# Optimization experiments

Hardware: AMD Instinct MI355X
Metric: run time of the kernel (lower is better)

Reference implementation:

```python
import jax, jax.numpy as jnp
import numpy as np

EMBED_DIM = 768
NUM_HEADS = 12
HEAD_DIM = EMBED_DIM // NUM_HEADS
SCALE = HEAD_DIM ** -0.5


def setup_inputs() -> dict:
    key = jax.random.key(0)
    k1, k2, k3, k4, k5 = jax.random.split(key, 5)
    B, T = 8, 1024
    init = 0.02
    return {
        "hidden_states": jax.random.normal(k1, (B, T, EMBED_DIM), dtype=jnp.float32),
        "qkv_w": jax.random.normal(k2, (EMBED_DIM, 3 * EMBED_DIM), dtype=jnp.float32) * init,
        "qkv_b": jnp.zeros((3 * EMBED_DIM,), dtype=jnp.float32),
        "proj_w": jax.random.normal(k3, (EMBED_DIM, EMBED_DIM), dtype=jnp.float32) * init,
        "proj_b": jnp.zeros((EMBED_DIM,), dtype=jnp.float32),
    }


def reference(hidden_states, qkv_w, qkv_b, proj_w, proj_b):
    B, T, E = hidden_states.shape
    # fused QKV projection: [B, T, 3E] -> [3, B, H, T, Dh]
    mixed = hidden_states @ qkv_w + qkv_b
    mixed = mixed.reshape(B, T, 3, NUM_HEADS, HEAD_DIM).transpose(2, 0, 3, 1, 4)
    q, k, v = mixed[0], mixed[1], mixed[2]
    # scores: [B, H, T, T]
    scores = jnp.einsum("bhqd,bhkd->bhqk", q, k) * SCALE
    probs = jax.nn.softmax(scores, axis=-1)
    # context: [B, T, H, Dh] -> [B, T, E]
    ctx = jnp.einsum("bhqk,bhkd->bqhd", probs, v).reshape(B, T, E)
    return ctx @ proj_w + proj_b
```

## Files before the change

### kernel.cpp

```cpp
#include <hip/hip_runtime.h>
#include <hip/hip_bf16.h>

#define B_ 8
#define T_ 1024
#define E_ 768
#define H_ 12
#define DH_ 64
#define E3_ 2304
#define M_ (B_ * T_)
#define SCALE_LOG2E 0.18033688011112042f

typedef __attribute__((ext_vector_type(8))) short short8;
typedef __attribute__((ext_vector_type(4))) float float4_;
typedef __attribute__((ext_vector_type(4))) unsigned short ushort4_;

__device__ __forceinline__ unsigned short f2bf(float f) {
    union { float f; unsigned int u; } v; v.f = f;
    unsigned int r = v.u + 0x7fffu + ((v.u >> 16) & 1u);
    return (unsigned short)(r >> 16);
}

__device__ __forceinline__ unsigned int pk_bf16(float a, float b) {
    float2 t; t.x = a; t.y = b;
    union { __hip_bfloat162 h; unsigned int u; } cv;
    cv.h = __float22bfloat162_rn(t);
    return cv.u;
}

__device__ __forceinline__ void gld_lds16(const unsigned short* g, unsigned short* l) {
    __builtin_amdgcn_global_load_lds(
        (const __attribute__((address_space(1))) void*)g,
        (__attribute__((address_space(3))) void*)l,
        16, 0, 0);
}

__global__ __launch_bounds__(256) void prep(const float* __restrict__ hs,
                                            const float* __restrict__ qkv_w,
                                            const float* __restrict__ proj_w,
                                            unsigned short* __restrict__ hs_bf,
                                            unsigned short* __restrict__ qkvwT,
                                            unsigned short* __restrict__ projwT) {
    __shared__ float tile[32][33];
    const int id = blockIdx.x;
    const int tid = threadIdx.x;
    if (id < 6144) {
        const int i = (id * 256 + tid) * 4;
        float4_ v = *(const float4_*)(hs + i);
        ushort4_ o;
        o.x = f2bf(v.x); o.y = f2bf(v.y); o.z = f2bf(v.z); o.w = f2bf(v.w);
        *(ushort4_*)(hs_bf + i) = o;
        return;
    }
    const float* W; unsigned short* Wt; int N, bx, by;
    if (id < 6144 + 1728) {
        const int t = id - 6144; W = qkv_w; Wt = qkvwT; N = E3_;
        bx = t % 72; by = t / 72;
    } else {
        const int t = id - 7872; W = proj_w; Wt = projwT; N = E_;
        bx = t % 24; by = t / 24;
    }
    const int k0 = by * 32, n0 = bx * 32;
    const int tx = tid & 31, ty = tid >> 5;
    for (int i = ty; i < 32; i += 8)
        tile[i][tx] = W[(size_t)(k0 + i) * N + n0 + tx];
    __syncthreads();
    for (int i = ty; i < 32; i += 8)
        Wt[(size_t)(n0 + i) * E_ + k0 + tx] = f2bf(tile[tx][i]);
}

__global__ __launch_bounds__(512, 2) void gemm288(const unsigned short* __restrict__ A,
                                                  const unsigned short* __restrict__ Wt,
                                                  const float* __restrict__ bias,
                                                  unsigned short* __restrict__ mixedOut,
                                                  unsigned short* __restrict__ Vt) {
    const int K = 768;
    const int NT = 12;
    __shared__ __align__(16) unsigned short lds[70144];

    const int tid = threadIdx.x;
    const int lane = tid & 63;
    const int w = tid >> 6;
    const int quad = lane >> 4;
    const int l16 = lane & 15;
    const int wM = w >> 1;
    const int wN = w & 1;

    const int id = blockIdx.x;
    const int xcd = id & 7;
    const int slot = id >> 3;
    const int bx = slot >> 2;
    const int byl = slot & 3;
    const int bm = (xcd * 4 + byl) * 256;
    const int bn = bx * 288;

    const int j4 = (w < 4) ? (w + 32) : 36;
    int kk0 = ((w % 18) / 6) * 64 + w;
    int kk1 = (((w + 8) % 18) / 6) * 64 + (w + 8);
    int kk2 = (((w + 16) % 18) / 6) * 64 + (w + 16);
    int kk3 = (((w + 24) % 18) / 6) * 64 + (w + 24);
    int kk4 = (j4 >= 36) ? (3 * 64 + 36) : (((j4 % 18) / 6) * 64 + j4);
#define CS_(a, b) { int _lo = min(a, b), _hi = max(a, b); a = _lo; b = _hi; }
    CS_(kk0, kk1) CS_(kk3, kk4) CS_(kk2, kk4) CS_(kk2, kk3) CS_(kk1, kk4)
    CS_(kk0, kk3) CS_(kk0, kk2) CS_(kk1, kk3) CS_(kk1, kk2)
#undef CS_
    const int b0 = kk0 & 63, b1 = kk1 & 63, b2 = kk2 & 63, b3 = kk3 & 63, b4 = kk4 & 63;

    const int srcrow = lane >> 3;
    const int ssw = ((lane & 7) ^ (srcrow & 7)) << 3;
    const unsigned short* gaL = A + (size_t)(bm + srcrow) * K + ssw;
    const unsigned short* gbL = Wt + (size_t)(bn + srcrow) * K + ssw;
    unsigned short* ldsl = lds + lane * 8;

    const int rsw0 = ((quad) ^ (l16 & 7)) << 3;
    const int rsw1 = ((quad + 4) ^ (l16 & 7)) << 3;
    const unsigned short* rdA = lds + (wM * 64 + l16) * 64;
    const unsigned short* rdB = lds + 32768 + (wN * 144 + l16) * 64;

    short8 aF[4][2], bF[3][2];
    float4_ acc[4][9] = {};

#define STA_(aj, toff, bufA) gld_lds16(gaL + (size_t)(aj) * 6144 + (toff), (bufA) + (aj) * 512)
#define STB_(j, toff, bufB) { \
    const int _j = (j); \
    const unsigned short* _s = gbL + (size_t)(_j >= 36 ? 0 : _j) * 6144 + (toff); \
    unsigned short* _d = (_j >= 36) ? (ldsl + 69632) : ((bufB) + _j * 512); \
    gld_lds16(_s, _d); }

#define LDA_(buf) { \
    const unsigned short* _a = rdA + (buf) * 16384; \
    aF[0][0] = *(const short8*)(_a + rsw0);        aF[0][1] = *(const short8*)(_a + rsw1); \
    aF[1][0] = *(const short8*)(_a + 1024 + rsw0); aF[1][1] = *(const short8*)(_a + 1024 + rsw1); \
    aF[2][0] = *(const short8*)(_a + 2048 + rsw0); aF[2][1] = *(const short8*)(_a + 2048 + rsw1); \
    aF[3][0] = *(const short8*)(_a + 3072 + rsw0); aF[3][1] = *(const short8*)(_a + 3072 + rsw1); }

#define LDB_(buf, nh) { \
    const unsigned short* _b = rdB + (buf) * 18432 + (nh) * 3072; \
    bF[0][0] = *(const short8*)(_b + rsw0);        bF[0][1] = *(const short8*)(_b + rsw1); \
    bF[1][0] = *(const short8*)(_b + 1024 + rsw0); bF[1][1] = *(const short8*)(_b + 1024 + rsw1); \
    bF[2][0] = *(const short8*)(_b + 2048 + rsw0); bF[2][1] = *(const short8*)(_b + 2048 + rsw1); }

#define MMA_(nh) \
    __builtin_amdgcn_s_setprio(1); \
    _Pragma("unroll") for (int mt = 0; mt < 4; ++mt) \
    _Pragma("unroll") for (int nt = 0; nt < 3; ++nt) { \
        acc[mt][(nh) * 3 + nt] = __builtin_amdgcn_mfma_f32_16x16x32_bf16( \
            aF[mt][0], bF[nt][0], acc[mt][(nh) * 3 + nt], 0, 0, 0); \
        acc[mt][(nh) * 3 + nt] = __builtin_amdgcn_mfma_f32_16x16x32_bf16( \
            aF[mt][1], bF[nt][1], acc[mt][(nh) * 3 + nt], 0, 0, 0); } \
    __builtin_amdgcn_s_setprio(0);

#define BARRIER_ __builtin_amdgcn_s_barrier()
#define WLGKM0_ { asm volatile("s_waitcnt lgkmcnt(0)" ::: "memory"); __builtin_amdgcn_sched_barrier(0); }
#define WVM3_ asm volatile("s_waitcnt vmcnt(3)" ::: "memory")
#define WVM0_ asm volatile("s_waitcnt vmcnt(0)" ::: "memory")

    {
        unsigned short* bufA = ldsl;
        unsigned short* bufB = ldsl + 32768;
        STA_(w, 0, bufA); STA_(w + 8, 0, bufA); STA_(w + 16, 0, bufA); STA_(w + 24, 0, bufA);
        STB_(b0, 0, bufB); STB_(b1, 0, bufB); STB_(b2, 0, bufB); STB_(b3, 0, bufB); STB_(b4, 0, bufB);
    }
    WVM3_; BARRIER_;

#pragma unroll 1
    for (int t = 0; t < NT - 1; ++t) {
        const int buf = t & 1;
        const int toff = (t + 1) * 64;
        unsigned short* bufA = ldsl + (buf ^ 1) * 16384;
        unsigned short* bufB = ldsl + 32768 + (buf ^ 1) * 18432;

        LDA_(buf); LDB_(buf, 0);
        STA_(w, toff, bufA); STA_(w + 8, toff, bufA); STA_(w + 16, toff, bufA);
        BARRIER_; WLGKM0_; MMA_(0);
        WVM3_; BARRIER_;
        LDB_(buf, 1);
        STA_(w + 24, toff, bufA); STB_(b0, toff, bufB); STB_(b1, toff, bufB);
        BARRIER_; WLGKM0_; MMA_(1);
        WVM3_; BARRIER_;
        LDB_(buf, 2);
        STB_(b2, toff, bufB); STB_(b3, toff, bufB); STB_(b4, toff, bufB);
        BARRIER_; WLGKM0_; MMA_(2);
        WVM3_; BARRIER_;
    }
    {
        LDA_(1); LDB_(1, 0);
        BARRIER_; WLGKM0_; MMA_(0);
        WVM0_; BARRIER_;
        LDB_(1, 1);
        BARRIER_; WLGKM0_; MMA_(1);
        BARRIER_;
        LDB_(1, 2);
        BARRIER_; WLGKM0_; MMA_(2);
    }
#undef STA_
#undef STB_
#undef LDA_
#undef LDB_
#undef MMA_

    const int bb = bm >> 10;
    const int tloc = (bm & 1023) + wM * 64;
#pragma unroll
    for (int ntg = 0; ntg < 9; ++ntg) {
        const int col = bn + wN * 144 + ntg * 16 + l16;
        const float bv = bias[col];
        if (col >= 1536) {
            const int n = col - 1536;
            const int h = n >> 6, d = n & 63;
            const size_t vrow = (size_t)((bb * H_ + h) * 64 + d) * T_;
#pragma unroll
            for (int mt = 0; mt < 4; ++mt) {
                uint2 pk;
                pk.x = pk_bf16(acc[mt][ntg][0] + bv, acc[mt][ntg][1] + bv);
                pk.y = pk_bf16(acc[mt][ntg][2] + bv, acc[mt][ntg][3] + bv);
                *(uint2*)(Vt + vrow + tloc + mt * 16 + quad * 4) = pk;
            }
        } else {
            const float qs = (col < 768) ? SCALE_LOG2E : 1.0f;
#pragma unroll
            for (int mt = 0; mt < 4; ++mt) {
#pragma unroll
                for (int i = 0; i < 4; ++i) {
                    const int row = bm + wM * 64 + mt * 16 + quad * 4 + i;
                    mixedOut[(size_t)row * E3_ + col] = f2bf((acc[mt][ntg][i] + bv) * qs);
                }
            }
        }
    }
}

__global__ __launch_bounds__(512, 2) void proj96(const unsigned short* __restrict__ A,
                                                 const unsigned short* __restrict__ Wt,
                                                 const float* __restrict__ bias,
                                                 float* __restrict__ out) {
    const int K = 768;
    const int NT = 12;
    __shared__ __align__(16) unsigned short lds[45568];

    const int tid = threadIdx.x;
    const int lane = tid & 63;
    const int w = tid >> 6;
    const int quad = lane >> 4;
    const int l16 = lane & 15;
    const int wM = w >> 1;
    const int wN = w & 1;

    const int id = blockIdx.x;
    const int xcd = id & 7;
    const int slot = id >> 3;
    const int bx = slot >> 2;
    const int byl = slot & 3;
    const int bm = (xcd * 4 + byl) * 256;
    const int bn = bx * 96;

    const int jB2 = (w < 4) ? (8 + w) : -1;

    const int srcrow = lane >> 3;
    const int ssw = ((lane & 7) ^ (srcrow & 7)) << 3;
    const unsigned short* gaL = A + (size_t)(bm + srcrow) * K + ssw;
    const unsigned short* gbL = Wt + (size_t)(bn + srcrow) * K + ssw;
    unsigned short* ldsl = lds + lane * 8;

    const int rsw0 = ((quad) ^ (l16 & 7)) << 3;
    const int rsw1 = ((quad + 4) ^ (l16 & 7)) << 3;
    const unsigned short* rdA = lds + (wM * 64 + l16) * 64;
    const unsigned short* rdB = lds + 32768 + (wN * 48 + l16) * 64;

    short8 aF[4][2], bF[2];
    float4_ acc[4][3] = {};

#define PSTA(aj, toff, nb) gld_lds16(gaL + (size_t)(aj) * 6144 + (toff), \
                                     ldsl + (nb) * 16384 + (aj) * 512)
#define PSTB(j, toff, nb) { \
    const int _j = (j); \
    const unsigned short* _s = gbL + (size_t)(_j < 0 ? 0 : _j) * 6144 + (toff); \
    unsigned short* _d = (_j < 0) ? (ldsl + 45056) : (ldsl + 32768 + (nb) * 6144 + _j * 512); \
    gld_lds16(_s, _d); }
#define PLDA(buf) { \
    const unsigned short* _a = rdA + (buf) * 16384; \
    aF[0][0] = *(const short8*)(_a + rsw0);        aF[0][1] = *(const short8*)(_a + rsw1); \
    aF[1][0] = *(const short8*)(_a + 1024 + rsw0); aF[1][1] = *(const short8*)(_a + 1024 + rsw1); \
    aF[2][0] = *(const short8*)(_a + 2048 + rsw0); aF[2][1] = *(const short8*)(_a + 2048 + rsw1); \
    aF[3][0] = *(const short8*)(_a + 3072 + rsw0); aF[3][1] = *(const short8*)(_a + 3072 + rsw1); }
#define PLDB(buf, nt_) { \
    const unsigned short* _b = rdB + (buf) * 6144 + (nt_) * 1024; \
    bF[0] = *(const short8*)(_b + rsw0); \
    bF[1] = *(const short8*)(_b + rsw1); }
#define PMMA(nt_) \
    __builtin_amdgcn_s_setprio(1); \
    _Pragma("unroll") for (int mt = 0; mt < 4; ++mt) { \
        acc[mt][nt_] = __builtin_amdgcn_mfma_f32_16x16x32_bf16(aF[mt][0], bF[0], acc[mt][nt_], 0, 0, 0); \
        acc[mt][nt_] = __builtin_amdgcn_mfma_f32_16x16x32_bf16(aF[mt][1], bF[1], acc[mt][nt_], 0, 0, 0); } \
    __builtin_amdgcn_s_setprio(0);
#define PBAR __builtin_amdgcn_s_barrier()
#define PLGKM0 { asm volatile("s_waitcnt lgkmcnt(0)" ::: "memory"); __builtin_amdgcn_sched_barrier(0); }

    PSTA(w, 0, 0); PSTA(w + 8, 0, 0); PSTA(w + 16, 0, 0); PSTA(w + 24, 0, 0);
    PSTB(w, 0, 0); PSTB(jB2, 0, 0);
    asm volatile("s_waitcnt vmcnt(0)" ::: "memory");
    PBAR;

#pragma unroll 1
    for (int t = 0; t < NT - 1; ++t) {
        const int buf = t & 1;
        const int nb = buf ^ 1;
        const int toff = (t + 1) * 64;

        PLDA(buf); PLDB(buf, 0);
        PSTA(w, toff, nb); PSTA(w + 8, toff, nb); PSTA(w + 16, toff, nb);
        PBAR; PLGKM0; PMMA(0);
        asm volatile("s_waitcnt vmcnt(3)" ::: "memory"); PBAR;
        PLDB(buf, 1);
        PSTA(w + 24, toff, nb); PSTB(w, toff, nb); PSTB(jB2, toff, nb);
        PBAR; PLGKM0; PMMA(1);
        asm volatile("s_waitcnt vmcnt(3)" ::: "memory"); PBAR;
        PLDB(buf, 2);
        PBAR; PLGKM0; PMMA(2);
        asm volatile("s_waitcnt vmcnt(0)" ::: "memory"); PBAR;
    }
    {
        PLDA(1);
        PLDB(1, 0); PLGKM0; PMMA(0);
        PLDB(1, 1); PLGKM0; PMMA(1);
        PLDB(1, 2); PLGKM0; PMMA(2);
    }
#undef PSTA
#undef PSTB
#undef PLDA
#undef PLDB
#undef PMMA
#undef PBAR
#undef PLGKM0

#pragma unroll
    for (int nt = 0; nt < 3; ++nt) {
        const int col = bn + wN * 48 + nt * 16 + l16;
        const float bv = bias[col];
#pragma unroll
        for (int mt = 0; mt < 4; ++mt) {
#pragma unroll
            for (int i = 0; i < 4; ++i) {
                const int row = bm + wM * 64 + mt * 16 + quad * 4 + i;
                out[(size_t)row * E_ + col] = acc[mt][nt][i] + bv;
            }
        }
    }
}

__global__ __launch_bounds__(256) void attn_mfma(const unsigned short* __restrict__ mixed,
                                                 const unsigned short* __restrict__ Vt,
                                                 unsigned short* __restrict__ ctx) {
    const int bh = blockIdx.x;
    const int b = bh / H_;
    const int h = bh % H_;
    const int q0 = blockIdx.y * 128;
    const int tid = threadIdx.x;
    const int lane = tid & 63;
    const int w = tid >> 6;
    const int quad = lane >> 4;
    const int l16 = lane & 15;

    __shared__ __align__(16) unsigned short Kl[8 * 520];
    __shared__ __align__(16) unsigned short Vl[8 * 520];
    __shared__ __align__(16) unsigned short Pl[4][32 * 72];
    unsigned short* pw = &Pl[w][0];

    short8 qf[2][2];
#pragma unroll
    for (int hh = 0; hh < 2; ++hh) {
        const size_t qrow = (size_t)(b * T_ + q0 + w * 32 + hh * 16 + l16) * E3_ + h * 64;
        qf[hh][0] = *(const short8*)(mixed + qrow + quad * 8);
        qf[hh][1] = *(const short8*)(mixed + qrow + 32 + quad * 8);
    }

    float4_ o[2][4] = {};
    float lps[2] = {0.0f, 0.0f};

    const size_t kbase = (size_t)(b * T_) * E3_ + E_ + h * 64;
    const size_t vtb = (size_t)bh * 64 * T_;

    const int srow = tid >> 3;
    const int sc = tid & 7;

    short8 k1 = *(const short8*)(mixed + kbase + (size_t)srow * E3_ + sc * 8);
    short8 k2 = *(const short8*)(mixed + kbase + (size_t)(srow + 32) * E3_ + sc * 8);
    short8 v1 = *(const short8*)(Vt + vtb + (size_t)srow * T_ + sc * 8);
    short8 v2 = *(const short8*)(Vt + vtb + (size_t)(srow + 32) * T_ + sc * 8);

    for (int kv0 = 0; kv0 < T_; kv0 += 64) {
        __syncthreads();
        *(short8*)(&Kl[sc * 520 + srow * 8]) = k1;
        *(short8*)(&Kl[sc * 520 + (srow + 32) * 8]) = k2;
        *(short8*)(&Vl[sc * 520 + srow * 8]) = v1;
        *(short8*)(&Vl[sc * 520 + (srow + 32) * 8]) = v2;
        __syncthreads();

        if (kv0 + 64 < T_) {
            const int kn = kv0 + 64;
            k1 = *(const short8*)(mixed + kbase + (size_t)(kn + srow) * E3_ + sc * 8);
            k2 = *(const short8*)(mixed + kbase + (size_t)(kn + srow + 32) * E3_ + sc * 8);
            v1 = *(const short8*)(Vt + vtb + (size_t)srow * T_ + kn + sc * 8);
            v2 = *(const short8*)(Vt + vtb + (size_t)(srow + 32) * T_ + kn + sc * 8);
        }

        float4_ st[2][4];
#pragma unroll
        for (int nt = 0; nt < 4; ++nt) {
            const int key = nt * 16 + l16;
            short8 kf0 = *(const short8*)(&Kl[quad * 520 + key * 8]);
            short8 kf1 = *(const short8*)(&Kl[(4 + quad) * 520 + key * 8]);
#pragma unroll
            for (int hh = 0; hh < 2; ++hh) {
                float4_ z = {};
                z = __builtin_amdgcn_mfma_f32_16x16x32_bf16(kf0, qf[hh][0], z, 0, 0, 0);
                st[hh][nt] = __builtin_amdgcn_mfma_f32_16x16x32_bf16(kf1, qf[hh][1], z, 0, 0, 0);
            }
        }

#pragma unroll
        for (int hh = 0; hh < 2; ++hh) {
#pragma unroll
            for (int nt = 0; nt < 4; ++nt) {
                const float p0 = __builtin_amdgcn_exp2f(st[hh][nt][0]);
                const float p1 = __builtin_amdgcn_exp2f(st[hh][nt][1]);
                const float p2 = __builtin_amdgcn_exp2f(st[hh][nt][2]);
                const float p3 = __builtin_amdgcn_exp2f(st[hh][nt][3]);
                uint2 pk;
                pk.x = pk_bf16(p0, p1);
                pk.y = pk_bf16(p2, p3);
                lps[hh] += (p0 + p1) + (p2 + p3);
                *(uint2*)(&pw[(hh * 16 + l16) * 72 + nt * 16 + quad * 4]) = pk;
            }
        }

        short8 pf[2][2];
#pragma unroll
        for (int hh = 0; hh < 2; ++hh) {
            pf[hh][0] = *(const short8*)(&pw[(hh * 16 + l16) * 72 + quad * 8]);
            pf[hh][1] = *(const short8*)(&pw[(hh * 16 + l16) * 72 + 32 + quad * 8]);
        }

#pragma unroll
        for (int dt = 0; dt < 4; ++dt) {
            const int d = dt * 16 + l16;
            short8 vf0 = *(const short8*)(&Vl[quad * 520 + d * 8]);
            short8 vf1 = *(const short8*)(&Vl[(4 + quad) * 520 + d * 8]);
#pragma unroll
            for (int hh = 0; hh < 2; ++hh) {
                o[hh][dt] = __builtin_amdgcn_mfma_f32_16x16x32_bf16(pf[hh][0], vf0, o[hh][dt], 0, 0, 0);
                o[hh][dt] = __builtin_amdgcn_mfma_f32_16x16x32_bf16(pf[hh][1], vf1, o[hh][dt], 0, 0, 0);
            }
        }
    }

#pragma unroll
    for (int hh = 0; hh < 2; ++hh) {
        float l = lps[hh];
        l += __shfl_xor(l, 16, 64);
        l += __shfl_xor(l, 32, 64);
        float4_ inv;
#pragma unroll
        for (int i = 0; i < 4; ++i)
            inv[i] = 1.0f / __shfl(l, quad * 4 + i, 16);
#pragma unroll
        for (int dt = 0; dt < 4; ++dt) {
#pragma unroll
            for (int i = 0; i < 4; ++i) {
                const float v = o[hh][dt][i] * inv[i];
                const size_t row = (size_t)(b * T_ + q0 + w * 32 + hh * 16 + quad * 4 + i);
                ctx[row * E_ + h * 64 + dt * 16 + l16] = f2bf(v);
            }
        }
    }
}

extern "C" void kernel_launch(void* const* d_in, const int* in_sizes, int n_in,
                              void* d_out, int out_size, void* d_ws, size_t ws_size,
                              hipStream_t stream) {
    const float* hs     = (const float*)d_in[0];
    const float* qkv_w  = (const float*)d_in[1];
    const float* qkv_b  = (const float*)d_in[2];
    const float* proj_w = (const float*)d_in[3];
    const float* proj_b = (const float*)d_in[4];
    float* out = (float*)d_out;

    unsigned short* hs_bf  = (unsigned short*)d_ws;
    unsigned short* qkvwT  = hs_bf + (size_t)M_ * E_;
    unsigned short* projwT = qkvwT + (size_t)E3_ * E_;
    unsigned short* mixed  = projwT + (size_t)E_ * E_;
    unsigned short* Vt     = mixed + (size_t)M_ * E3_;
    unsigned short* ctx    = hs_bf;

    prep<<<8448, 256, 0, stream>>>(hs, qkv_w, proj_w, hs_bf, qkvwT, projwT);

    gemm288<<<256, 512, 0, stream>>>(hs_bf, qkvwT, qkv_b, mixed, Vt);
    attn_mfma<<<dim3(B_ * H_, T_ / 128), 256, 0, stream>>>(mixed, Vt, ctx);
    proj96<<<256, 512, 0, stream>>>(ctx, projwT, proj_b, out);
}
```

Before: 176.6 us.

## Double-buffer K/V tiles in shared memory with one barrier per iteration

Splits the K and V shared-memory tiles into two buffers. Each iteration computes on the current buffer while storing the next tile into the other buffer and prefetching the tile after that into registers. This removes one of the two __syncthreads per iteration and lets LDS writes overlap compute. The cost is twice the LDS for K/V, which may lower occupancy, plus extra register pressure from the deeper prefetch.

```diff
diff --git a/kernel.cpp b/kernel.cpp
--- a/kernel.cpp
+++ b/kernel.cpp
@@ -360,8 +360,8 @@
     const int quad = lane >> 4;
     const int l16 = lane & 15;
 
-    __shared__ __align__(16) unsigned short Kl[8 * 520];
-    __shared__ __align__(16) unsigned short Vl[8 * 520];
+    __shared__ __align__(16) unsigned short Kl[2][8 * 520];
+    __shared__ __align__(16) unsigned short Vl[2][8 * 520];
     __shared__ __align__(16) unsigned short Pl[4][32 * 72];
     unsigned short* pw = &Pl[w][0];
 
@@ -382,21 +382,38 @@
     const int srow = tid >> 3;
     const int sc = tid & 7;
 
-    short8 k1 = *(const short8*)(mixed + kbase + (size_t)srow * E3_ + sc * 8);
-    short8 k2 = *(const short8*)(mixed + kbase + (size_t)(srow + 32) * E3_ + sc * 8);
-    short8 v1 = *(const short8*)(Vt + vtb + (size_t)srow * T_ + sc * 8);
-    short8 v2 = *(const short8*)(Vt + vtb + (size_t)(srow + 32) * T_ + sc * 8);
-
-    for (int kv0 = 0; kv0 < T_; kv0 += 64) {
-        __syncthreads();
-        *(short8*)(&Kl[sc * 520 + srow * 8]) = k1;
-        *(short8*)(&Kl[sc * 520 + (srow + 32) * 8]) = k2;
-        *(short8*)(&Vl[sc * 520 + srow * 8]) = v1;
-        *(short8*)(&Vl[sc * 520 + (srow + 32) * 8]) = v2;
-        __syncthreads();
-
-        if (kv0 + 64 < T_) {
-            const int kn = kv0 + 64;
+    {
+        short8 a1 = *(const short8*)(mixed + kbase + (size_t)srow * E3_ + sc * 8);
+        short8 a2 = *(const short8*)(mixed + kbase + (size_t)(srow + 32) * E3_ + sc * 8);
+        short8 a3 = *(const short8*)(Vt + vtb + (size_t)srow * T_ + sc * 8);
+        short8 a4 = *(const short8*)(Vt + vtb + (size_t)(srow + 32) * T_ + sc * 8);
+        *(short8*)(&Kl[0][sc * 520 + srow * 8]) = a1;
+        *(short8*)(&Kl[0][sc * 520 + (srow + 32) * 8]) = a2;
+        *(short8*)(&Vl[0][sc * 520 + srow * 8]) = a3;
+        *(short8*)(&Vl[0][sc * 520 + (srow + 32) * 8]) = a4;
+    }
+    short8 k1 = *(const short8*)(mixed + kbase + (size_t)(64 + srow) * E3_ + sc * 8);
+    short8 k2 = *(const short8*)(mixed + kbase + (size_t)(64 + srow + 32) * E3_ + sc * 8);
+    short8 v1 = *(const short8*)(Vt + vtb + (size_t)srow * T_ + 64 + sc * 8);
+    short8 v2 = *(const short8*)(Vt + vtb + (size_t)(srow + 32) * T_ + 64 + sc * 8);
+    __syncthreads();
+
+#pragma unroll 1
+    for (int t = 0; t < 16; ++t) {
+        const int cur = t & 1;
+        const unsigned short* kl = &Kl[cur][0];
+        const unsigned short* vl = &Vl[cur][0];
+
+        if (t + 1 < 16) {
+            unsigned short* kd = &Kl[cur ^ 1][0];
+            unsigned short* vd = &Vl[cur ^ 1][0];
+            *(short8*)(&kd[sc * 520 + srow * 8]) = k1;
+            *(short8*)(&kd[sc * 520 + (srow + 32) * 8]) = k2;
+            *(short8*)(&vd[sc * 520 + srow * 8]) = v1;
+            *(short8*)(&vd[sc * 520 + (srow + 32) * 8]) = v2;
+        }
+        if (t + 2 < 16) {
+            const int kn = (t + 2) * 64;
             k1 = *(const short8*)(mixed + kbase + (size_t)(kn + srow) * E3_ + sc * 8);
             k2 = *(const short8*)(mixed + kbase + (size_t)(kn + srow + 32) * E3_ + sc * 8);
             v1 = *(const short8*)(Vt + vtb + (size_t)srow * T_ + kn + sc * 8);
@@ -407,8 +424,8 @@
 #pragma unroll
         for (int nt = 0; nt < 4; ++nt) {
             const int key = nt * 16 + l16;
-            short8 kf0 = *(const short8*)(&Kl[quad * 520 + key * 8]);
-            short8 kf1 = *(const short8*)(&Kl[(4 + quad) * 520 + key * 8]);
+            short8 kf0 = *(const short8*)(&kl[quad * 520 + key * 8]);
+            short8 kf1 = *(const short8*)(&kl[(4 + quad) * 520 + key * 8]);
 #pragma unroll
             for (int hh = 0; hh < 2; ++hh) {
                 float4_ z = {};
@@ -443,14 +460,16 @@
 #pragma unroll
         for (int dt = 0; dt < 4; ++dt) {
             const int d = dt * 16 + l16;
-            short8 vf0 = *(const short8*)(&Vl[quad * 520 + d * 8]);
-            short8 vf1 = *(const short8*)(&Vl[(4 + quad) * 520 + d * 8]);
+            short8 vf0 = *(const short8*)(&vl[quad * 520 + d * 8]);
+            short8 vf1 = *(const short8*)(&vl[(4 + quad) * 520 + d * 8]);
 #pragma unroll
             for (int hh = 0; hh < 2; ++hh) {
                 o[hh][dt] = __builtin_amdgcn_mfma_f32_16x16x32_bf16(pf[hh][0], vf0, o[hh][dt], 0, 0, 0);
                 o[hh][dt] = __builtin_amdgcn_mfma_f32_16x16x32_bf16(pf[hh][1], vf1, o[hh][dt], 0, 0, 0);
             }
         }
+
+        if (t + 1 < 16) __syncthreads();
     }
 
 #pragma unroll
```

Measured after the change: 177.2 us. No clear change (+0.3%).
